# Optimization experiments

Hardware: AMD Instinct MI355X
Metric: run time of the kernel (lower is better)

## Reference

```python
import jax, jax.numpy as jnp
import numpy as np
import math

D = 1024
H = 16
DH = D // H
B = 4
NSEQ = 1024
NSEG = 2
EXP = 4


def layer_norm(x, w, b=None, eps=1e-5):
    mu = jnp.mean(x, axis=-1, keepdims=True)
    var = jnp.mean((x - mu) ** 2, axis=-1, keepdims=True)
    y = (x - mu) * jax.lax.rsqrt(var + eps) * w
    return y + b if b is not None else y


def apply_rope(x, positions):
    # x: [B, L, H, Dh]; ESM-style rotate-half RoPE
    dh = x.shape[-1]
    inv_freq = 1.0 / (10000.0 ** (jnp.arange(0, dh, 2, dtype=jnp.float32) / dh))
    freqs = positions.astype(jnp.float32)[:, None] * inv_freq[None, :]  # [L, Dh/2]
    emb = jnp.concatenate([freqs, freqs], axis=-1)  # [L, Dh]
    cos = jnp.cos(emb)[None, :, None, :]
    sin = jnp.sin(emb)[None, :, None, :]
    x1, x2 = jnp.split(x, 2, axis=-1)
    return x * cos + jnp.concatenate([-x2, x1], axis=-1) * sin


def timestep_embedding(timesteps, embedding_dim=256, max_len=10000):
    # timesteps: [N]
    ts = timesteps * max_len
    half = embedding_dim // 2
    emb = math.log(max_len) / (half - 1)
    freqs = jnp.exp(jnp.arange(half, dtype=jnp.float32) * -emb)
    e = ts.astype(jnp.float32)[:, None] * freqs[None, :]
    return jnp.concatenate([jnp.sin(e), jnp.cos(e)], axis=1)  # [N, 256]


def make_autoregressive_attn_mask(batch_mask, n_seg):
    b, n_res = batch_mask.shape
    L = (n_seg + 1) * n_res
    causal = jnp.tril(jnp.ones((L, L), dtype=bool))[None, None]  # [1,1,L,L]
    tiled = jnp.tile(batch_mask, (1, n_seg + 1)).astype(bool)  # [B, L]
    key_valid = tiled[:, None, None, :]
    q_valid = tiled[:, None, :, None]
    allowed = causal & key_valid & q_valid  # [B,1,L,L]
    first_edit = (batch_mask[:, None, :] * batch_mask[:, :, None]).astype(bool)
    allowed = allowed.at[:, 0, :n_res, :n_res].set(first_edit)
    return allowed


def setup_inputs() -> dict:
    key = jax.random.key(0)
    ks = jax.random.split(key, 32)
    s = 0.02
    p = lambda i, shape: jax.random.normal(ks[i], shape, dtype=jnp.float32) * s
    inp = {
        'x_seq': jax.random.normal(ks[0], (B, NSEQ, D), dtype=jnp.float32),
        'x_struc': jax.random.normal(ks[1], (B, 1, D), dtype=jnp.float32),
        'temp': jax.random.uniform(ks[2], (B, 1, 1), dtype=jnp.float32),
        'mask': jnp.ones((B, NSEQ), dtype=jnp.float32),
        'ln_qs_w': jnp.ones((D,), jnp.float32), 'ln_qs_b': jnp.zeros((D,), jnp.float32),
        'W_qkv_seq': p(3, (D, 3 * D)),
        'ln_qt_w': jnp.ones((D,), jnp.float32), 'ln_qt_b': jnp.zeros((D,), jnp.float32),
        'W_qkv_struc': p(4, (D, 3 * D)),
        'q_ln_seq_w': jnp.ones((D,), jnp.float32), 'k_ln_seq_w': jnp.ones((D,), jnp.float32),
        'q_ln_struc_w': jnp.ones((D,), jnp.float32), 'k_ln_struc_w': jnp.ones((D,), jnp.float32),
        'W_out_seq': p(5, (D, D)), 'W_out_struc': p(6, (D, D)),
        'temp_w1': p(7, (1, D)), 'temp_b1': jnp.zeros((D,), jnp.float32),
        'temp_w2': p(8, (D, D)), 'temp_b2': jnp.zeros((D,), jnp.float32),
        'T_w1': p(9, (256, D)), 'T_b1': jnp.zeros((D,), jnp.float32),
        'T_w2': p(10, (D, D)), 'T_b2': jnp.zeros((D,), jnp.float32),
        'ffn_seq_ln_w': jnp.ones((D,), jnp.float32), 'ffn_seq_ln_b': jnp.zeros((D,), jnp.float32),
        'ffn_seq_w1': p(11, (D, EXP * D)), 'ffn_seq_w2': p(12, (EXP * D, D)),
        'ffn_struc_ln_w': jnp.ones((D,), jnp.float32), 'ffn_struc_ln_b': jnp.zeros((D,), jnp.float32),
        'ffn_struc_w1': p(13, (D, EXP * D)), 'ffn_struc_w2': p(14, (EXP * D, D)),
        'T': 1,
    }
    return inp


def reference(x_seq, x_struc, temp, mask,
              ln_qs_w, ln_qs_b, W_qkv_seq,
              ln_qt_w, ln_qt_b, W_qkv_struc,
              q_ln_seq_w, k_ln_seq_w, q_ln_struc_w, k_ln_struc_w,
              W_out_seq, W_out_struc,
              temp_w1, temp_b1, temp_w2, temp_b2,
              T_w1, T_b1, T_w2, T_b2,
              ffn_seq_ln_w, ffn_seq_ln_b, ffn_seq_w1, ffn_seq_w2,
              ffn_struc_ln_w, ffn_struc_ln_b, ffn_struc_w1, ffn_struc_w2,
              T):
    b, n_seq, d = x_seq.shape
    n_seg, index = NSEG, 0  # index=0 prefill path

    # --- seq track QKV (index == 0 only) ---
    qkv_seq = layer_norm(x_seq, ln_qs_w, ln_qs_b) @ W_qkv_seq
    q_s, k_s, v_s = jnp.split(qkv_seq, 3, axis=-1)
    q_s = layer_norm(q_s, q_ln_seq_w)
    k_s = layer_norm(k_s, k_ln_seq_w)
    pos_seq = jnp.arange(n_seq)
    q_s = apply_rope(q_s.reshape(b, n_seq, H, DH), pos_seq).reshape(b, n_seq, d)
    k_s = apply_rope(k_s.reshape(b, n_seq, H, DH), pos_seq).reshape(b, n_seq, d)

    # --- struc track conditioning + QKV ---
    position_T = jnp.arange(n_seg, dtype=jnp.float32) * T / 100.0
    T_input = jnp.repeat(position_T, n_seq)[index:index + 1]  # [1]
    x_norm = layer_norm(x_struc, ln_qt_w, ln_qt_b)
    temp_e = jax.nn.silu(temp @ temp_w1 + temp_b1) @ temp_w2 + temp_b2  # [B,1,D]
    t_emb = timestep_embedding(T_input)  # [1,256]
    T_e = jax.nn.silu(t_emb @ T_w1 + T_b1) @ T_w2 + T_b2  # [1,D]
    x_mod = x_norm + temp_e + T_e[None, :, :]
    qkv_t = x_mod @ W_qkv_struc
    q_t, k_t, v_t = jnp.split(qkv_t, 3, axis=-1)
    q_t = layer_norm(q_t, q_ln_struc_w)
    k_t = layer_norm(k_t, k_ln_struc_w)
    pos_res = jnp.tile(jnp.arange(n_seq), n_seg)[index:index + 1]  # [1]
    q_t = apply_rope(q_t.reshape(b, 1, H, DH), pos_res).reshape(b, 1, d)
    k_t = apply_rope(k_t.reshape(b, 1, H, DH), pos_res).reshape(b, 1, d)

    # --- KV cache contents for index 0: [seq tokens, struc token] ---
    keys = jnp.concatenate([k_s, k_t], axis=1)    # [B, N_seq+1, D]
    values = jnp.concatenate([v_s, v_t], axis=1)
    queries = jnp.concatenate([q_s, q_t], axis=1)

    to_heads = lambda t: t.reshape(b, -1, H, DH).transpose(0, 2, 1, 3)  # b h s d
    qh, kh, vh = to_heads(queries), to_heads(keys), to_heads(values)

    allowed = make_autoregressive_attn_mask(mask, n_seg)  # [B,1,L,L]
    Lq = n_seq + index + 1
    attn_mask = allowed[:, :, :Lq, :Lq]

    scale = 1.0 / math.sqrt(DH)
    scores = jnp.einsum('bhqd,bhkd->bhqk', qh, kh) * scale
    scores = jnp.where(attn_mask, scores, -1e9)
    probs = jax.nn.softmax(scores, axis=-1)
    ctx = jnp.einsum('bhqk,bhkd->bhqd', probs, vh)
    ctx = ctx.transpose(0, 2, 1, 3).reshape(b, Lq, d)

    out_seq = ctx[:, :n_seq] @ W_out_seq
    out_struc = ctx[:, n_seq:] @ W_out_struc

    # residuals (scaling_factor = 1)
    x_seq = x_seq + out_seq
    x_struc = x_struc + out_struc

    # GELU FFNs (LN -> Linear -> GELU -> Linear, no bias)
    h_seq = jax.nn.gelu(layer_norm(x_seq, ffn_seq_ln_w, ffn_seq_ln_b) @ ffn_seq_w1, approximate=False) @ ffn_seq_w2
    x_seq = x_seq + h_seq
    h_struc = jax.nn.gelu(layer_norm(x_struc, ffn_struc_ln_w, ffn_struc_ln_b) @ ffn_struc_w1, approximate=False) @ ffn_struc_w2
    x_struc = x_struc + h_struc

    return (x_seq, x_struc)
```

## Files before the change

kernel.cpp:

```cpp
#include <hip/hip_runtime.h>

typedef __attribute__((ext_vector_type(8))) short short8;
typedef __attribute__((ext_vector_type(4))) float f32x4;
typedef __attribute__((ext_vector_type(4))) unsigned short us4;

#define DEV static __device__ __forceinline__

DEV float bf2f(unsigned short u){ union{unsigned u; float f;} v; v.u=((unsigned)u)<<16; return v.f; }
DEV unsigned short f2bf(float f){ union{float f; unsigned u;} v; v.f=f; unsigned r=v.u+0x7fffu+((v.u>>16)&1u); return (unsigned short)(r>>16); }
DEV float gelu_f(float x){ return 0.5f*x*(1.0f+erff(x*0.7071067811865475f)); }
DEV float silu_f(float x){ return x/(1.0f+__expf(-x)); }

DEV void gload16(const void* g, void* l){
  __builtin_amdgcn_global_load_lds((const __attribute__((address_space(1))) void*)g,
                                   (__attribute__((address_space(3))) void*)l, 16, 0, 0);
}

DEV void blk_reduce2(float &a, float &b){
  #pragma unroll
  for (int off=32; off>0; off>>=1){ a += __shfl_down(a,off); b += __shfl_down(b,off); }
  __shared__ float sa[4], sb[4];
  int w=threadIdx.x>>6;
  if((threadIdx.x&63)==0){ sa[w]=a; sb[w]=b; }
  __syncthreads();
  a=sa[0]+sa[1]+sa[2]+sa[3]; b=sb[0]+sb[1]+sb[2]+sb[3];
}

template<int OUTF32>
__global__ __launch_bounds__(256) void ln_rows(const float* __restrict__ x,
    const float* __restrict__ w, const float* __restrict__ bias, void* __restrict__ outp)
{
  int row=blockIdx.x, t=threadIdx.x;
  const float* xr = x + (size_t)row*1024;
  float4 v = *(const float4*)(xr + t*4);
  float s=v.x+v.y+v.z+v.w;
  float s2=v.x*v.x+v.y*v.y+v.z*v.z+v.w*v.w;
  blk_reduce2(s,s2);
  float mu=s*(1.0f/1024.0f);
  float rs=rsqrtf(s2*(1.0f/1024.0f)-mu*mu+1e-5f);
  int d0=t*4;
  const float* vp=(const float*)&v;
  float y[4];
  #pragma unroll
  for(int j=0;j<4;j++){ float bb = bias? bias[d0+j] : 0.0f; y[j]=(vp[j]-mu)*rs*w[d0+j]+bb; }
  if (OUTF32){
    float4 o; o.x=y[0];o.y=y[1];o.z=y[2];o.w=y[3];
    *(float4*)((float*)outp + (size_t)row*1024 + d0) = o;
  } else {
    us4 o;
    #pragma unroll
    for(int j=0;j<4;j++) o[j]=f2bf(y[j]);
    *(us4*)((unsigned short*)outp + (size_t)row*1024 + d0) = o;
  }
}

__global__ __launch_bounds__(256) void wtrans(const float* __restrict__ Bm,
    unsigned short* __restrict__ Bt, int K, int N)
{
  __shared__ float tile[32][33];
  int nb = blockIdx.x*32, kb = blockIdx.y*32;
  int tx = threadIdx.x&31, ty = threadIdx.x>>5;
  #pragma unroll
  for(int i=0;i<32;i+=8) tile[ty+i][tx] = Bm[(size_t)(kb+ty+i)*N + nb+tx];
  __syncthreads();
  #pragma unroll
  for(int i=0;i<32;i+=8) Bt[(size_t)(nb+ty+i)*K + kb+tx] = f2bf(tile[tx][ty+i]);
}

__global__ __launch_bounds__(256) void vtrans(const unsigned short* __restrict__ qkv,
    unsigned short* __restrict__ vT)
{
  __shared__ unsigned short tile[32][33];
  int d0 = blockIdx.x*32, tk0 = blockIdx.y*32, b = blockIdx.z;
  int tx = threadIdx.x&31, ty = threadIdx.x>>5;
  #pragma unroll
  for(int i=0;i<32;i+=8) tile[ty+i][tx] = qkv[(size_t)(b*1024+tk0+ty+i)*3072 + 2048 + d0+tx];
  __syncthreads();
  #pragma unroll
  for(int i=0;i<32;i+=8) vT[(size_t)(b*1024+d0+ty+i)*1024 + tk0+tx] = tile[tx][ty+i];
}

__global__ void rope_table(float* __restrict__ tab){
  int idx = blockIdx.x*256 + threadIdx.x;
  if (idx >= 1024*32) return;
  int pos = idx>>5, i = idx&31;
  float inv = exp2f(-(float)i * (13.287712379549449f/32.0f));
  float a = (float)pos*inv;
  tab[idx*2]   = cosf(a);
  tab[idx*2+1] = sinf(a);
}

__global__ __launch_bounds__(256) void qk_ln_rope(
    const unsigned short* __restrict__ qkv, const float* __restrict__ qw, const float* __restrict__ kw,
    const float* __restrict__ tab, unsigned short* __restrict__ qr, unsigned short* __restrict__ kr)
{
  __shared__ float lnr[1024];
  int row=blockIdx.x, part=blockIdx.y, t=threadIdx.x;
  const unsigned short* src = qkv + (size_t)row*3072 + part*1024 + t*4;
  us4 u = *(const us4*)src;
  float x[4];
  #pragma unroll
  for(int j=0;j<4;j++) x[j]=bf2f(u[j]);
  float s=x[0]+x[1]+x[2]+x[3];
  float s2=x[0]*x[0]+x[1]*x[1]+x[2]*x[2]+x[3]*x[3];
  blk_reduce2(s,s2);
  float mu=s*(1.0f/1024.0f);
  float rsg=rsqrtf(s2*(1.0f/1024.0f)-mu*mu+1e-5f);
  const float* w = part? kw : qw;
  int d0=t*4;
  #pragma unroll
  for(int j=0;j<4;j++) lnr[d0+j]=(x[j]-mu)*rsg*w[d0+j];
  __syncthreads();
  int n = row & 1023;
  unsigned short* dst = (part? kr: qr) + (size_t)row*1024 + d0;
  us4 o;
  #pragma unroll
  for(int j=0;j<4;j++){
    int d=d0+j, dh=d&63, fi=dh&31;
    float c=tab[(n*32+fi)*2], sn=tab[(n*32+fi)*2+1];
    float p=lnr[d^32];
    o[j]=f2bf(lnr[d]*c + ((dh<32)? -p : p)*sn);
  }
  *(us4*)dst = o;
}

template<int EPI>
__global__ __launch_bounds__(256) void gemm_bt(
    const unsigned short* __restrict__ A, int lda,
    const unsigned short* __restrict__ Bt, int ldb,
    int N, int K, void* Cout, const float* resp)
{
  __shared__ unsigned short As[8192];
  __shared__ unsigned short Bs[8192];
  const int t=threadIdx.x;
  int GX=gridDim.x, GY=gridDim.y, nwg=GX*GY;
  int m0, n0;
  if (!((GX&7) || (nwg&63))){
    int d = blockIdx.y*GX + blockIdx.x;
    int xcd = d&7, j = d>>3;
    int g = xcd*(nwg>>3) + j;
    int chunk = g>>6, local = g&63;
    int chunks_x = GX>>3;
    int cx = chunk%chunks_x, cy = chunk/chunks_x;
    n0 = (cx*8 + (local&7))*128;
    m0 = (cy*8 + (local>>3))*128;
  } else {
    m0 = blockIdx.y*128; n0 = blockIdx.x*128;
  }
  const int kofs = blockIdx.z*K;
  const int l=t&63, w=t>>6, lg=l>>4, lr=l&15;
  const int wm=(w>>1)*64, wn=(w&1)*64;
  const int srow=t>>3, sseg=(t&7)^(srow&7);
  const f32x4 z4 = {0.f,0.f,0.f,0.f};
  f32x4 acc[4][4];
  #pragma unroll
  for(int i=0;i<4;i++)
    #pragma unroll
    for(int j=0;j<4;j++) acc[i][j]=z4;
  for (int k0=0;k0<K;k0+=64){
    __syncthreads();
    #pragma unroll
    for(int i=0;i<4;i++){
      gload16(A  + (size_t)(m0+srow+i*32)*lda + kofs + k0 + sseg*8, As + w*512 + i*2048);
      gload16(Bt + (size_t)(n0+srow+i*32)*ldb + kofs + k0 + sseg*8, Bs + w*512 + i*2048);
    }
    __syncthreads();
    #pragma unroll
    for(int ks=0;ks<2;ks++){
      short8 a[4], bfr[4];
      #pragma unroll
      for(int m=0;m<4;m++){
        int row=wm+m*16+lr;
        a[m] = *(const short8*)&As[row*64 + ((ks*4+lg)^(row&7))*8];
      }
      #pragma unroll
      for(int n=0;n<4;n++){
        int row=wn+n*16+lr;
        bfr[n] = *(const short8*)&Bs[row*64 + ((ks*4+lg)^(row&7))*8];
      }
      #pragma unroll
      for(int m=0;m<4;m++)
        #pragma unroll
        for(int n=0;n<4;n++)
          acc[m][n] = __builtin_amdgcn_mfma_f32_16x16x32_bf16(a[m], bfr[n], acc[m][n], 0,0,0);
    }
  }
  #pragma unroll
  for(int m=0;m<4;m++){
    #pragma unroll
    for(int n=0;n<4;n++){
      #pragma unroll
      for(int r=0;r<4;r++){
        int row=m0+wm+m*16+lg*4+r, col=n0+wn+n*16+lr;
        size_t idx=(size_t)row*N+col;
        float v=acc[m][n][r];
        if (EPI==1){ ((float*)Cout)[idx] = v + resp[idx]; }
        else if (EPI==2){ ((unsigned short*)Cout)[idx] = f2bf(gelu_f(v)); }
        else if (EPI==3){ atomicAdd((float*)Cout + idx, v); }
        else { ((unsigned short*)Cout)[idx] = f2bf(v); }
      }
    }
  }
}

__global__ __launch_bounds__(256) void flash_seq(
    const unsigned short* __restrict__ qr, const unsigned short* __restrict__ kr,
    const unsigned short* __restrict__ vT, unsigned short* __restrict__ ctx)
{
  __shared__ unsigned short Pl[4][32][64];
  const int t=threadIdx.x, w=t>>6, l=t&63, lg=l>>4, lr=l&15;
  int d = blockIdx.y*gridDim.x + blockIdx.x;
  int xcd = d&7;
  int g = xcd*64 + (d>>3);
  const int bh = g>>3, b = bh>>4, h = bh&15;
  const int q0 = (g&7)*128;
  const f32x4 z4 = {0.f,0.f,0.f,0.f};
  short8 qf[2][2];
  #pragma unroll
  for(int mf=0;mf<2;mf++)
    #pragma unroll
    for(int ks=0;ks<2;ks++)
      qf[mf][ks] = *(const short8*)(qr + (size_t)(b*1024 + q0 + w*32 + mf*16 + lr)*1024 + h*64 + ks*32 + lg*8);
  f32x4 o[2][4];
  float m_[2][4], l_[2][4];
  #pragma unroll
  for(int mf=0;mf<2;mf++){
    #pragma unroll
    for(int nd=0;nd<4;nd++) o[mf][nd]=z4;
    #pragma unroll
    for(int r=0;r<4;r++){ m_[mf][r]=-1e30f; l_[mf][r]=0.f; }
  }
  for (int kv0=0;kv0<1024;kv0+=64){
    f32x4 s[2][4];
    #pragma unroll
    for(int mf=0;mf<2;mf++)
      #pragma unroll
      for(int nf=0;nf<4;nf++) s[mf][nf]=z4;
    #pragma unroll
    for(int ks=0;ks<2;ks++){
      #pragma unroll
      for(int nf=0;nf<4;nf++){
        short8 kf = *(const short8*)(kr + (size_t)(b*1024+kv0+nf*16+lr)*1024 + h*64 + ks*32 + lg*8);
        s[0][nf] = __builtin_amdgcn_mfma_f32_16x16x32_bf16(qf[0][ks], kf, s[0][nf],0,0,0);
        s[1][nf] = __builtin_amdgcn_mfma_f32_16x16x32_bf16(qf[1][ks], kf, s[1][nf],0,0,0);
      }
    }
    #pragma unroll
    for(int mf=0;mf<2;mf++)
      #pragma unroll
      for(int nf=0;nf<4;nf++) s[mf][nf] = s[mf][nf]*0.125f;
    #pragma unroll
    for(int mf=0;mf<2;mf++){
      #pragma unroll
      for(int r=0;r<4;r++){
        float mx = fmaxf(fmaxf(s[mf][0][r],s[mf][1][r]),fmaxf(s[mf][2][r],s[mf][3][r]));
        #pragma unroll
        for(int off=8;off>0;off>>=1) mx = fmaxf(mx, __shfl_xor(mx,off));
        float mn = fmaxf(m_[mf][r], mx);
        float f  = __expf(m_[mf][r]-mn);
        float rs = 0.f;
        #pragma unroll
        for(int nf=0;nf<4;nf++){ float p=__expf(s[mf][nf][r]-mn); s[mf][nf][r]=p; rs+=p; }
        #pragma unroll
        for(int off=8;off>0;off>>=1) rs += __shfl_xor(rs,off);
        l_[mf][r]=l_[mf][r]*f+rs; m_[mf][r]=mn;
        #pragma unroll
        for(int nd=0;nd<4;nd++) o[mf][nd][r]*=f;
      }
    }
    #pragma unroll
    for(int mf=0;mf<2;mf++)
      #pragma unroll
      for(int nf=0;nf<4;nf++)
        #pragma unroll
        for(int r=0;r<4;r++){
          int prow = mf*16+lg*4+r;
          int col = (((nf*2+(lr>>3)) ^ (prow&7))<<3) + (lr&7);
          Pl[w][prow][col] = f2bf(s[mf][nf][r]);
        }
    #pragma unroll
    for(int ks2=0;ks2<2;ks2++){
      short8 pa0 = *(const short8*)&Pl[w][lr]   [((ks2*4+lg)^(lr&7))<<3];
      short8 pa1 = *(const short8*)&Pl[w][16+lr][((ks2*4+lg)^(lr&7))<<3];
      #pragma unroll
      for(int nd=0;nd<4;nd++){
        short8 vf = *(const short8*)(vT + (size_t)(b*1024 + h*64 + nd*16+lr)*1024 + kv0 + ks2*32 + lg*8);
        o[0][nd] = __builtin_amdgcn_mfma_f32_16x16x32_bf16(pa0, vf, o[0][nd],0,0,0);
        o[1][nd] = __builtin_amdgcn_mfma_f32_16x16x32_bf16(pa1, vf, o[1][nd],0,0,0);
      }
    }
  }
  #pragma unroll
  for(int mf=0;mf<2;mf++){
    #pragma unroll
    for(int r=0;r<4;r++){
      float inv = 1.0f/l_[mf][r];
      #pragma unroll
      for(int nd=0;nd<4;nd++){
        ctx[(size_t)(b*1024 + q0 + w*32 + mf*16 + lg*4 + r)*1024 + h*64 + nd*16 + lr]
          = f2bf(o[mf][nd][r]*inv);
      }
    }
  }
}

__global__ __launch_bounds__(256) void struc_prep_a(const float* __restrict__ T_w1, float* __restrict__ sTacc){
  int j = blockIdx.x*256+threadIdx.x;
  float u=0.f;
  #pragma unroll
  for(int i=0;i<16;i++) u += T_w1[(size_t)(128+blockIdx.y*16+i)*1024 + j];
  atomicAdd(&sTacc[j], u);
}

__global__ __launch_bounds__(256) void struc_prep_b(const float* __restrict__ temp,
    const float* __restrict__ temp_w1, const float* __restrict__ temp_b1,
    const float* __restrict__ T_b1, const float* __restrict__ sTacc,
    float* __restrict__ sT, float* __restrict__ stemp)
{
  int j = blockIdx.x*256+threadIdx.x;
  sT[j] = silu_f(sTacc[j]+T_b1[j]);
  #pragma unroll
  for(int b=0;b<4;b++){ float z = temp[b]*temp_w1[j]+temp_b1[j]; stemp[b*1024+j]=silu_f(z); }
}

__global__ __launch_bounds__(256) void struc_xmod(const float* __restrict__ xs,
    const float* __restrict__ qtw, const float* __restrict__ qtb,
    const float* __restrict__ eacc, const float* __restrict__ tacc,
    const float* __restrict__ temp_b2, const float* __restrict__ T_b2, float* __restrict__ xmod)
{
  int b=blockIdx.x, t=threadIdx.x;
  float4 v = *(const float4*)(xs + (size_t)b*1024 + t*4);
  float s=v.x+v.y+v.z+v.w, s2=v.x*v.x+v.y*v.y+v.z*v.z+v.w*v.w;
  blk_reduce2(s,s2);
  float mu=s*(1.0f/1024.0f);
  float rs=rsqrtf(s2*(1.0f/1024.0f)-mu*mu+1e-5f);
  const float* vp=(const float*)&v;
  #pragma unroll
  for(int j=0;j<4;j++){
    int d=t*4+j;
    xmod[b*1024+d] = (vp[j]-mu)*rs*qtw[d] + qtb[d] + eacc[b*1024+d] + tacc[d] + T_b2[d] + temp_b2[d];
  }
}

template<int MR>
__global__ __launch_bounds__(256) void smallm_part(
    const float* __restrict__ A, const float* __restrict__ Bm,
    float* __restrict__ accp, int K, int N)
{
  __shared__ float As[MR][64];
  const int t=threadIdx.x;
  const int n = blockIdx.x*256 + t;
  const int k0 = blockIdx.y*64;
  if (t < MR*64){ int m=t>>6, kk=t&63; As[m][kk]=A[(size_t)m*K + k0+kk]; }
  __syncthreads();
  float acc[MR];
  #pragma unroll
  for(int m=0;m<MR;m++) acc[m]=0.f;
  #pragma unroll 8
  for(int kk=0;kk<64;kk++){
    float wv = Bm[(size_t)(k0+kk)*N + n];
    #pragma unroll
    for(int m=0;m<MR;m++) acc[m] += As[m][kk]*wv;
  }
  #pragma unroll
  for(int m=0;m<MR;m++) atomicAdd(&accp[(size_t)m*N + n], acc[m]);
}

__global__ __launch_bounds__(256) void gelu_vec(const float* __restrict__ in, float* __restrict__ out, int n){
  int i = blockIdx.x*256+threadIdx.x;
  if (i<n) out[i]=gelu_f(in[i]);
}

__global__ __launch_bounds__(256) void struc_qk_ln(float* qkv_t,
    const float* __restrict__ qw, const float* __restrict__ kw)
{
  int b=blockIdx.x>>1, part=blockIdx.x&1, t=threadIdx.x;
  float* xr = qkv_t + (size_t)b*3072 + part*1024;
  float4 v = *(const float4*)(xr + t*4);
  float s=v.x+v.y+v.z+v.w, s2=v.x*v.x+v.y*v.y+v.z*v.z+v.w*v.w;
  blk_reduce2(s,s2);
  float mu=s*(1.0f/1024.0f);
  float rsg=rsqrtf(s2*(1.0f/1024.0f)-mu*mu+1e-5f);
  const float* w = part? kw : qw;
  const float* vp=(const float*)&v;
  #pragma unroll
  for(int j=0;j<4;j++) xr[t*4+j]=(vp[j]-mu)*rsg*w[t*4+j];
}

__global__ __launch_bounds__(256) void struc_attn_part(
    const float* __restrict__ qkv_t, const unsigned short* __restrict__ kr,
    const unsigned short* __restrict__ qkv, float* __restrict__ part)
{
  __shared__ float qs[64];
  __shared__ float pb[4][64];
  const int bh=blockIdx.x, b=bh>>4, h=bh&15;
  const int t=threadIdx.x, w=t>>6, l=t&63;
  if (t<64) qs[t]=qkv_t[(size_t)b*3072 + h*64 + t];
  __syncthreads();
  const int key = blockIdx.y*256 + w*64 + l;
  const unsigned short* krow = kr + (size_t)(b*1024+key)*1024 + h*64;
  float s=0.f;
  #pragma unroll
  for(int j=0;j<8;j++){
    short8 kk = *(const short8*)(krow + j*8);
    #pragma unroll
    for(int e=0;e<8;e++) s += qs[j*8+e]*bf2f((unsigned short)kk[e]);
  }
  s *= 0.125f;
  float mx=s;
  #pragma unroll
  for(int off=32;off>0;off>>=1) mx=fmaxf(mx,__shfl_xor(mx,off));
  float p=__expf(s-mx);
  float ls=p;
  #pragma unroll
  for(int off=32;off>0;off>>=1) ls+=__shfl_xor(ls,off);
  pb[w][l]=p;
  const int k0 = blockIdx.y*256 + w*64;
  float cacc=0.f;
  for(int k2=0;k2<64;k2++)
    cacc += pb[w][k2]*bf2f(qkv[(size_t)(b*1024+k0+k2)*3072 + 2048 + h*64 + l]);
  float* pp = part + ((size_t)bh*16 + blockIdx.y*4 + w)*66;
  if(l==0){ pp[0]=mx; pp[1]=ls; }
  pp[2+l]=cacc;
}

__global__ __launch_bounds__(64) void struc_attn_comb(
    const float* __restrict__ part, const float* __restrict__ qkv_t, float* __restrict__ ctx_t)
{
  const int bh=blockIdx.x, b=bh>>4, h=bh&15, l=threadIdx.x;
  float M=-1e30f;
  #pragma unroll
  for(int i=0;i<16;i++) M=fmaxf(M, part[((size_t)bh*16+i)*66]);
  float lsum=0.f, cacc=0.f;
  #pragma unroll
  for(int i=0;i<16;i++){
    const float* pp = part + ((size_t)bh*16+i)*66;
    float f=__expf(pp[0]-M);
    lsum += pp[1]*f;
    cacc += pp[2+l]*f;
  }
  float qd=qkv_t[(size_t)b*3072 + h*64 + l];
  float kd=qkv_t[(size_t)b*3072 + 1024 + h*64 + l];
  float prod=qd*kd;
  #pragma unroll
  for(int off=32;off>0;off>>=1) prod+=__shfl_xor(prod,off);
  float st=prod*0.125f;
  float M2=fmaxf(M,st), fA=__expf(M-M2), pt=__expf(st-M2);
  cacc = cacc*fA + pt*qkv_t[(size_t)b*3072 + 2048 + h*64 + l];
  lsum = lsum*fA + pt;
  ctx_t[(size_t)b*1024 + h*64 + l] = cacc/lsum;
}

extern "C" void kernel_launch(void* const* d_in, const int* in_sizes, int n_in,
                              void* d_out, int out_size, void* d_ws, size_t ws_size,
                              hipStream_t stream){
  const float* x_seq    = (const float*)d_in[0];
  const float* x_struc  = (const float*)d_in[1];
  const float* temp     = (const float*)d_in[2];
  const float* ln_qs_w  = (const float*)d_in[4];
  const float* ln_qs_b  = (const float*)d_in[5];
  const float* W_qkv_seq= (const float*)d_in[6];
  const float* ln_qt_w  = (const float*)d_in[7];
  const float* ln_qt_b  = (const float*)d_in[8];
  const float* W_qkv_st = (const float*)d_in[9];
  const float* q_ln_seq_w=(const float*)d_in[10];
  const float* k_ln_seq_w=(const float*)d_in[11];
  const float* q_ln_st_w= (const float*)d_in[12];
  const float* k_ln_st_w= (const float*)d_in[13];
  const float* W_out_seq= (const float*)d_in[14];
  const float* W_out_st = (const float*)d_in[15];
  const float* temp_w1  = (const float*)d_in[16];
  const float* temp_b1  = (const float*)d_in[17];
  const float* temp_w2  = (const float*)d_in[18];
  const float* temp_b2  = (const float*)d_in[19];
  const float* T_w1     = (const float*)d_in[20];
  const float* T_b1     = (const float*)d_in[21];
  const float* T_w2     = (const float*)d_in[22];
  const float* T_b2     = (const float*)d_in[23];
  const float* ffn_s_ln_w=(const float*)d_in[24];
  const float* ffn_s_ln_b=(const float*)d_in[25];
  const float* ffn_s_w1 = (const float*)d_in[26];
  const float* ffn_s_w2 = (const float*)d_in[27];
  const float* ffn_t_ln_w=(const float*)d_in[28];
  const float* ffn_t_ln_b=(const float*)d_in[29];
  const float* ffn_t_w1 = (const float*)d_in[30];
  const float* ffn_t_w2 = (const float*)d_in[31];

  char* ws = (char*)d_ws;
  unsigned short* xn   = (unsigned short*)(ws + 0);
  unsigned short* qkv  = (unsigned short*)(ws + 8388608);
  unsigned short* qr   = (unsigned short*)(ws + 33554432);
  unsigned short* kr   = (unsigned short*)(ws + 41943040);
  unsigned short* ctx  = (unsigned short*)(ws + 50331648);
  float* tab   = (float*)(ws + 58720256);
  char* sm = ws + 58982400;
  float* sT    = (float*)(sm + 0);
  float* stemp = (float*)(sm + 4096);
  float* tacc  = (float*)(sm + 20544);
  float* eacc  = (float*)(sm + 24640);
  float* xmod  = (float*)(sm + 41024);
  float* qkvt  = (float*)(sm + 57408);
  float* ctxt  = (float*)(sm + 106560);
  float* xsn   = (float*)(sm + 122944);
  float* hs    = (float*)(sm + 139328);
  float* hsacc = (float*)(sm + 204864);
  float* part  = (float*)(sm + 270400);
  float* sTacc = (float*)(sm + 540800);
  unsigned short* wqkvT = (unsigned short*)(ws + 50331648);
  unsigned short* woutT = (unsigned short*)(ws + 33554432);
  unsigned short* ffn1T = (unsigned short*)(ws + 41943040);
  unsigned short* ffn2T = (unsigned short*)(ws + 50331648);
  unsigned short* vT   = xn;
  unsigned short* hbuf = qkv;
  float* outf = (float*)d_out;
  float* out_tail = outf + 4194304;

  ln_rows<0><<<4096,256,0,stream>>>(x_seq, ln_qs_w, ln_qs_b, xn);
  wtrans<<<dim3(96,32),256,0,stream>>>(W_qkv_seq, wqkvT, 1024, 3072);
  rope_table<<<128,256,0,stream>>>(tab);
  gemm_bt<0><<<dim3(24,32),256,0,stream>>>(xn, 1024, wqkvT, 1024, 3072, 1024, qkv, nullptr);
  vtrans<<<dim3(32,32,4),256,0,stream>>>(qkv, vT);
  qk_ln_rope<<<dim3(4096,2),256,0,stream>>>(qkv, q_ln_seq_w, k_ln_seq_w, tab, qr, kr);
  flash_seq<<<dim3(8,64),256,0,stream>>>(qr, kr, vT, ctx);
  hipMemsetAsync(sTacc, 0, 1024*4, stream);
  hipMemsetAsync(tacc, 0, 1024*4, stream);
  hipMemsetAsync(eacc, 0, 4096*4, stream);
  hipMemsetAsync(qkvt, 0, 12288*4, stream);
  struc_prep_a<<<dim3(4,8),256,0,stream>>>(T_w1, sTacc);
  struc_prep_b<<<4,256,0,stream>>>(temp, temp_w1, temp_b1, T_b1, sTacc, sT, stemp);
  smallm_part<1><<<dim3(4,16),256,0,stream>>>(sT, T_w2, tacc, 1024, 1024);
  smallm_part<4><<<dim3(4,16),256,0,stream>>>(stemp, temp_w2, eacc, 1024, 1024);
  struc_xmod<<<4,256,0,stream>>>(x_struc, ln_qt_w, ln_qt_b, eacc, tacc, temp_b2, T_b2, xmod);
  smallm_part<4><<<dim3(12,16),256,0,stream>>>(xmod, W_qkv_st, qkvt, 1024, 3072);
  struc_qk_ln<<<8,256,0,stream>>>(qkvt, q_ln_st_w, k_ln_st_w);
  struc_attn_part<<<dim3(64,4),256,0,stream>>>(qkvt, kr, qkv, part);
  struc_attn_comb<<<64,64,0,stream>>>(part, qkvt, ctxt);
  wtrans<<<dim3(32,32),256,0,stream>>>(W_out_seq, woutT, 1024, 1024);
  hipMemcpyAsync(outf, x_seq, (size_t)4194304*4, hipMemcpyDeviceToDevice, stream);
  gemm_bt<3><<<dim3(8,32,2),256,0,stream>>>(ctx, 1024, woutT, 1024, 1024, 512, outf, nullptr);
  hipMemcpyAsync(out_tail, x_struc, 4096*4, hipMemcpyDeviceToDevice, stream);
  smallm_part<4><<<dim3(4,16),256,0,stream>>>(ctxt, W_out_st, out_tail, 1024, 1024);
  ln_rows<0><<<4096,256,0,stream>>>(outf, ffn_s_ln_w, ffn_s_ln_b, xn);
  wtrans<<<dim3(128,32),256,0,stream>>>(ffn_s_w1, ffn1T, 1024, 4096);
  gemm_bt<2><<<dim3(32,32),256,0,stream>>>(xn, 1024, ffn1T, 1024, 4096, 1024, hbuf, nullptr);
  wtrans<<<dim3(32,128),256,0,stream>>>(ffn_s_w2, ffn2T, 4096, 1024);
  gemm_bt<3><<<dim3(8,32,4),256,0,stream>>>(hbuf, 4096, ffn2T, 4096, 1024, 1024, outf, nullptr);
  ln_rows<1><<<4,256,0,stream>>>(out_tail, ffn_t_ln_w, ffn_t_ln_b, xsn);
  hipMemsetAsync(hsacc, 0, 16384*4, stream);
  smallm_part<4><<<dim3(16,16),256,0,stream>>>(xsn, ffn_t_w1, hsacc, 1024, 4096);
  gelu_vec<<<64,256,0,stream>>>(hsacc, hs, 16384);
  smallm_part<4><<<dim3(4,64),256,0,stream>>>(hs, ffn_t_w2, out_tail, 4096, 1024);
  (void)in_sizes; (void)n_in; (void)out_size; (void)ws_size;
}
```

Baseline: 484.6 us.

## Add 256x256-tile GEMM for QKV/FFN1, fuse residual into out-proj, halve FFN2 split-K

Adds a new 512-thread GEMM kernel with 256x256 output tiles and an XCD-aware tile remap, and uses it for the QKV projection and the FFN first layer. Larger tiles give more operand reuse per LDS load and fewer workgroups. The out-projection now uses the EPI=1 residual epilogue reading x_seq directly with no split-K, which drops the device memcpy and the atomic accumulation. FFN2 split-K goes from 4 to 2. The cost is fewer workgroups (192/256) on a 256-CU part, so the grid fills at most one wave, and the large accumulator arrays raise register pressure.

```diff
diff --git a/kernel.cpp b/kernel.cpp
--- a/kernel.cpp
+++ b/kernel.cpp
@@ -122,6 +122,76 @@
     o[j]=f2bf(lnr[d]*c + ((dh<32)? -p : p)*sn);
   }
   *(us4*)dst = o;
+}
+
+template<int EPI>
+__global__ __launch_bounds__(512) void gemm256(
+    const unsigned short* __restrict__ A, int lda,
+    const unsigned short* __restrict__ Bt, int ldb,
+    int N, int K, void* Cout)
+{
+  __shared__ unsigned short As[16384];
+  __shared__ unsigned short Bs[16384];
+  const int t=threadIdx.x;
+  int GX=gridDim.x, GY=gridDim.y, nwg=GX*GY;
+  int bx, by;
+  if (!(nwg&7)){
+    int d = blockIdx.y*GX + blockIdx.x;
+    int g = (d&7)*(nwg>>3) + (d>>3);
+    bx = g%GX; by = g/GX;
+  } else { bx = blockIdx.x; by = blockIdx.y; }
+  const int m0=by*256, n0=bx*256;
+  const int l=t&63, w=t>>6, lg=l>>4, lr=l&15;
+  const int wr=w>>2, wc=w&3;
+  const int srow=t>>3, sseg=(t&7)^((t>>3)&7);
+  const f32x4 z4 = {0.f,0.f,0.f,0.f};
+  f32x4 acc[8][4];
+  #pragma unroll
+  for(int i=0;i<8;i++)
+    #pragma unroll
+    for(int j=0;j<4;j++) acc[i][j]=z4;
+  for (int k0=0;k0<K;k0+=64){
+    __syncthreads();
+    #pragma unroll
+    for(int i=0;i<4;i++){
+      gload16(A  + (size_t)(m0+srow+i*64)*lda + k0 + sseg*8, As + i*4096 + w*512);
+      gload16(Bt + (size_t)(n0+srow+i*64)*ldb + k0 + sseg*8, Bs + i*4096 + w*512);
+    }
+    __syncthreads();
+    #pragma unroll
+    for(int ks=0;ks<2;ks++){
+      short8 a[8], bfr[4];
+      #pragma unroll
+      for(int m=0;m<8;m++){
+        int row=wr*128+m*16+lr;
+        a[m] = *(const short8*)&As[row*64 + ((ks*4+lg)^(row&7))*8];
+      }
+      #pragma unroll
+      for(int n=0;n<4;n++){
+        int row=wc*64+n*16+lr;
+        bfr[n] = *(const short8*)&Bs[row*64 + ((ks*4+lg)^(row&7))*8];
+      }
+      #pragma unroll
+      for(int m=0;m<8;m++)
+        #pragma unroll
+        for(int n=0;n<4;n++)
+          acc[m][n] = __builtin_amdgcn_mfma_f32_16x16x32_bf16(a[m], bfr[n], acc[m][n], 0,0,0);
+    }
+  }
+  #pragma unroll
+  for(int m=0;m<8;m++){
+    #pragma unroll
+    for(int n=0;n<4;n++){
+      #pragma unroll
+      for(int r=0;r<4;r++){
+        int row=m0+wr*128+m*16+lg*4+r, col=n0+wc*64+n*16+lr;
+        size_t idx=(size_t)row*N+col;
+        float v=acc[m][n][r];
+        if (EPI==2){ ((unsigned short*)Cout)[idx] = f2bf(gelu_f(v)); }
+        else { ((unsigned short*)Cout)[idx] = f2bf(v); }
+      }
+    }
+  }
 }
 
 template<int EPI>
@@ -518,7 +588,7 @@
   ln_rows<0><<<4096,256,0,stream>>>(x_seq, ln_qs_w, ln_qs_b, xn);
   wtrans<<<dim3(96,32),256,0,stream>>>(W_qkv_seq, wqkvT, 1024, 3072);
   rope_table<<<128,256,0,stream>>>(tab);
-  gemm_bt<0><<<dim3(24,32),256,0,stream>>>(xn, 1024, wqkvT, 1024, 3072, 1024, qkv, nullptr);
+  gemm256<0><<<dim3(12,16),512,0,stream>>>(xn, 1024, wqkvT, 1024, 3072, 1024, qkv);
   vtrans<<<dim3(32,32,4),256,0,stream>>>(qkv, vT);
   qk_ln_rope<<<dim3(4096,2),256,0,stream>>>(qkv, q_ln_seq_w, k_ln_seq_w, tab, qr, kr);
   flash_seq<<<dim3(8,64),256,0,stream>>>(qr, kr, vT, ctx);
@@ -536,15 +606,14 @@
   struc_attn_part<<<dim3(64,4),256,0,stream>>>(qkvt, kr, qkv, part);
   struc_attn_comb<<<64,64,0,stream>>>(part, qkvt, ctxt);
   wtrans<<<dim3(32,32),256,0,stream>>>(W_out_seq, woutT, 1024, 1024);
-  hipMemcpyAsync(outf, x_seq, (size_t)4194304*4, hipMemcpyDeviceToDevice, stream);
-  gemm_bt<3><<<dim3(8,32,2),256,0,stream>>>(ctx, 1024, woutT, 1024, 1024, 512, outf, nullptr);
+  gemm_bt<1><<<dim3(8,32),256,0,stream>>>(ctx, 1024, woutT, 1024, 1024, 1024, outf, x_seq);
   hipMemcpyAsync(out_tail, x_struc, 4096*4, hipMemcpyDeviceToDevice, stream);
   smallm_part<4><<<dim3(4,16),256,0,stream>>>(ctxt, W_out_st, out_tail, 1024, 1024);
   ln_rows<0><<<4096,256,0,stream>>>(outf, ffn_s_ln_w, ffn_s_ln_b, xn);
   wtrans<<<dim3(128,32),256,0,stream>>>(ffn_s_w1, ffn1T, 1024, 4096);
-  gemm_bt<2><<<dim3(32,32),256,0,stream>>>(xn, 1024, ffn1T, 1024, 4096, 1024, hbuf, nullptr);
+  gemm256<2><<<dim3(16,16),512,0,stream>>>(xn, 1024, ffn1T, 1024, 4096, 1024, hbuf);
   wtrans<<<dim3(32,128),256,0,stream>>>(ffn_s_w2, ffn2T, 4096, 1024);
-  gemm_bt<3><<<dim3(8,32,4),256,0,stream>>>(hbuf, 4096, ffn2T, 4096, 1024, 1024, outf, nullptr);
+  gemm_bt<3><<<dim3(8,32,2),256,0,stream>>>(hbuf, 4096, ffn2T, 4096, 1024, 2048, outf, nullptr);
   ln_rows<1><<<4,256,0,stream>>>(out_tail, ffn_t_ln_w, ffn_t_ln_b, xsn);
   hipMemsetAsync(hsacc, 0, 16384*4, stream);
   smallm_part<4><<<dim3(16,16),256,0,stream>>>(xsn, ffn_t_w1, hsacc, 1024, 4096);
```

After: 451.5 us. 6.8% less time.
